# Performance work log

Hardware: AMD Instinct MI355X
Metric: run time of the kernel (lower is better)

Reference implementation:

```python
import jax, jax.numpy as jnp
import numpy as np

N_E, FEAT, REST = 2048, 512, 8
HEAD, LENGTH = 8, 64


def setup_inputs() -> dict:
    key = jax.random.key(0)
    kx, kq, kk, kd = jax.random.split(key, 4)
    x = jax.random.normal(kx, (N_E, FEAT, REST), dtype=jnp.float32)
    Q = jax.random.normal(kq, (HEAD, LENGTH, FEAT), dtype=jnp.float32)
    K = jax.random.normal(kk, (HEAD, LENGTH, FEAT), dtype=jnp.float32)
    D = jax.random.normal(kd, (HEAD, LENGTH, FEAT), dtype=jnp.float32)
    return {"x": x, "Q": Q, "K": K, "D": D}


def _linear(a, W):
    # a: (n, f, *rest), W: (h, q, f) -> y: (n, h, q, *rest)
    y = jnp.einsum('nf...,hqf->nhq...', a, W)
    # L2-normalize over the last 3 axes (here: h? no -- axes (q, rest...) per the
    # original code: sum over (-1,-2,-3) of (n,h,q,rest) = (h,q,rest) per n)
    norm = jnp.sqrt((y * y).sum((-1, -2, -3), keepdims=True))
    return y / norm


def reference(x, Q, K, D):
    n_e = x.shape[0]
    rest = x.shape[2:]
    head, length = Q.shape[0], Q.shape[1]
    q = _linear(x, Q)  # (n, h, l, rest)
    k = _linear(x, K)
    d = _linear(x, D)
    # scores over electrons: contract (l, rest) -> (h, n, n)
    w = jax.nn.softmax(jnp.einsum('nh...,mh...->hnm', q, k), axis=-1)
    # weighted combine: (h,n,m) x (m,h,l,rest) -> (n,h,l,rest)
    v = jnp.einsum('hnm,mhl...->nhl...', w, d)
    return v.reshape((n_e, head * length) + rest)
```

## Files before the change

kernel.cpp:

```cpp
#include <hip/hip_runtime.h>
#include <math.h>

#define NE   2048
#define FEAT 512

typedef short short8 __attribute__((ext_vector_type(8)));
typedef float f32x4  __attribute__((ext_vector_type(4)));

__device__ __forceinline__ unsigned short f2bf(float f) {
    union { float f; unsigned u; } v; v.f = f;
    unsigned r = v.u + 0x7fffu + ((v.u >> 16) & 1u);
    return (unsigned short)(r >> 16);
}
__device__ __forceinline__ float bf2f(unsigned b) {
    union { unsigned u; float f; } v; v.u = b << 16;
    return v.f;
}
__device__ __forceinline__ unsigned pack2(float a, float b) {
    return (unsigned)f2bf(a) | ((unsigned)f2bf(b) << 16);
}

__device__ __forceinline__ void gld16(unsigned short* lds, const unsigned short* g) {
    __builtin_amdgcn_global_load_lds(
        (const __attribute__((address_space(1))) unsigned int*)g,
        (__attribute__((address_space(3))) unsigned int*)lds,
        16, 0, 0);
}

__device__ __forceinline__ void bar() {
    asm volatile("" ::: "memory");
    __builtin_amdgcn_s_barrier();
    asm volatile("" ::: "memory");
}
#define VMW(n) asm volatile("s_waitcnt vmcnt(" #n ")" ::: "memory")


__global__ __launch_bounds__(256) void wconv_kernel(
    const float* __restrict__ Wq, const float* __restrict__ Wk, const float* __restrict__ Wd,
    unsigned short* __restrict__ wbf)
{
    const int t = threadIdx.x;
    const float* W = (blockIdx.y == 0) ? Wq : (blockIdx.y == 1) ? Wk : Wd;
    unsigned short* o = wbf + (size_t)blockIdx.y * 262144;
    const int idx = blockIdx.x * 2048 + t * 8;
    const float4* p = (const float4*)(W + idx);
    float4 v0 = p[0], v1 = p[1];
    *(uint4*)(o + idx) = make_uint4(pack2(v0.x, v0.y), pack2(v0.z, v0.w),
                                    pack2(v1.x, v1.y), pack2(v1.z, v1.w));
}

__global__ __launch_bounds__(256) void xpose_kernel(const float* __restrict__ x,
                                                    unsigned short* __restrict__ xt)
{
    __shared__ float xs[8 * 516];
    const int t = threadIdx.x;
    const int n = blockIdx.x;
    const float4* xp = (const float4*)(x + (size_t)n * 4096);
    #pragma unroll
    for (int i = 0; i < 4; ++i) {
        int idx = t + 256 * i;
        float4 v = xp[idx];
        int f = idx >> 1, rh = (idx & 1) * 4;
        xs[(rh + 0) * 516 + f] = v.x;
        xs[(rh + 1) * 516 + f] = v.y;
        xs[(rh + 2) * 516 + f] = v.z;
        xs[(rh + 3) * 516 + f] = v.w;
    }
    __syncthreads();
    const int r = t >> 5, f0 = (t & 31) * 16;
    const float* src = &xs[r * 516 + f0];
    unsigned o[8];
    #pragma unroll
    for (int j = 0; j < 8; ++j) o[j] = pack2(src[2 * j], src[2 * j + 1]);
    unsigned short* dst = xt + (size_t)n * 4096 + r * 512 + f0;
    *(uint4*)dst       = make_uint4(o[0], o[1], o[2], o[3]);
    *(uint4*)(dst + 8) = make_uint4(o[4], o[5], o[6], o[7]);
}

__global__ __launch_bounds__(512, 1) void proj_gemm(
    const unsigned short* __restrict__ wbf, const unsigned short* __restrict__ xt,
    unsigned short* __restrict__ qb, unsigned short* __restrict__ kb, unsigned short* __restrict__ db,
    float* __restrict__ s2)
{
    __shared__ unsigned short SM[49152];
    const int t = threadIdx.x;
    int bid = blockIdx.x + 128 * (blockIdx.y + 2 * blockIdx.z);
    int swz = (bid & 7) * 96 + (bid >> 3);
    const int bx = swz & 127, rest = swz >> 7;
    const int my = rest & 1, w = rest >> 1;
    const unsigned short* W = wbf + (size_t)w * 262144;
    unsigned short* out = (w == 0) ? qb : (w == 1) ? kb : db;
    const int M0 = my * 256;
    const int N0 = bx * 128;
    const int wave = t >> 6, lane = t & 63, quad = lane >> 4, l16 = lane & 15;
    const int wr = wave >> 1, wc = wave & 1;
    const int lrow = lane >> 3;
    const int scol = ((lane & 7) ^ lrow) * 8;

    f32x4 acc[4][4];
    #pragma unroll
    for (int m = 0; m < 4; ++m)
        #pragma unroll
        for (int n = 0; n < 4; ++n) acc[m][n] = {0.f, 0.f, 0.f, 0.f};

    auto STAGE = [&](int kc, int buf) {
        unsigned short* A = SM + buf * 16384;
        unsigned short* B = SM + 32768 + buf * 8192;
        #pragma unroll
        for (int p = 0; p < 4; ++p) {
            int c = p * 8 + wave;
            gld16(A + c * 512, W + (size_t)(M0 + c * 8 + lrow) * 512 + kc * 64 + scol);
        }
        #pragma unroll
        for (int p = 0; p < 2; ++p) {
            int c = p * 8 + wave;
            gld16(B + c * 512, xt + (size_t)(N0 + c * 8 + lrow) * 512 + kc * 64 + scol);
        }
    };
    auto COMPUTE = [&](int buf) {
        const unsigned short* A = SM + buf * 16384;
        const unsigned short* B = SM + 32768 + buf * 8192;
        #pragma unroll
        for (int kk = 0; kk < 2; ++kk) {
            int so = ((kk * 4 + quad) ^ (l16 & 7)) * 8;
            short8 a[4], b[4];
            #pragma unroll
            for (int m = 0; m < 4; ++m)
                a[m] = *(const short8*)&A[(wr * 64 + m * 16 + l16) * 64 + so];
            #pragma unroll
            for (int n = 0; n < 4; ++n)
                b[n] = *(const short8*)&B[(wc * 64 + n * 16 + l16) * 64 + so];
            #pragma unroll
            for (int m = 0; m < 4; ++m)
                #pragma unroll
                for (int n = 0; n < 4; ++n)
                    acc[m][n] = __builtin_amdgcn_mfma_f32_16x16x32_bf16(a[m], b[n], acc[m][n], 0, 0, 0);
        }
    };

    STAGE(0, 0);
    STAGE(1, 1);
    for (int kc = 0; kc < 8; ++kc) {
        if (kc < 7) { VMW(6); } else { VMW(0); }
        bar();
        COMPUTE(kc & 1);
        bar();
        if (kc + 2 < 8) STAGE(kc + 2, kc & 1);
    }

    float cs[4];
    #pragma unroll
    for (int n = 0; n < 4; ++n) {
        float s = 0.f;
        #pragma unroll
        for (int m = 0; m < 4; ++m)
            #pragma unroll
            for (int reg = 0; reg < 4; ++reg)
                s += acc[m][n][reg] * acc[m][n][reg];
        cs[n] = s;
    }
    #pragma unroll
    for (int n = 0; n < 4; ++n) {
        float s = cs[n];
        s += __shfl_xor(s, 16);
        s += __shfl_xor(s, 32);
        s += __shfl_xor(s, 1);
        s += __shfl_xor(s, 2);
        s += __shfl_xor(s, 4);
        if ((lane & 7) == 0 && lane < 16) {
            int n_elec = (N0 >> 3) + wc * 8 + n * 2 + (lane >> 3);
            atomicAdd(&s2[w * NE + n_elec], s);
        }
    }

    unsigned short* T = SM;
    #pragma unroll
    for (int m = 0; m < 4; ++m)
        #pragma unroll
        for (int reg = 0; reg < 4; ++reg) {
            int row = wr * 64 + m * 16 + quad * 4 + reg;
            #pragma unroll
            for (int n = 0; n < 4; ++n)
                T[row * 136 + wc * 64 + n * 16 + l16] = f2bf(acc[m][n][reg]);
        }
    __syncthreads();
    #pragma unroll
    for (int i = 0; i < 8; ++i) {
        int c = t + 512 * i;
        int row = c & 255, cb = c >> 8;
        uint4 v = *(const uint4*)(T + row * 136 + cb * 8);
        int hl = M0 + row;
        unsigned short* dst = out + (size_t)(hl >> 6) * 1048576 + (size_t)(hl & 63) * 8
                                  + (size_t)((N0 >> 3) + cb) * 512;
        *(uint4*)dst = v;
    }
}

__global__ __launch_bounds__(256) void sfinal_kernel(const float* __restrict__ s2,
                                                     float* __restrict__ scales)
{
    int i = blockIdx.x * 256 + threadIdx.x;
    scales[i] = rsqrtf(s2[i]);
}

__global__ __launch_bounds__(256) void dtrans_kernel(
    const unsigned short* __restrict__ db, const float* __restrict__ invd,
    unsigned short* __restrict__ dT)
{
    __shared__ float Ts[64 * 68];
    const int t = threadIdx.x;
    const int h = blockIdx.z, n0 = blockIdx.y * 64, f0 = blockIdx.x * 64;
    const int rr = t >> 3, cs = (t & 7) * 8;
    #pragma unroll
    for (int p = 0; p < 2; ++p) {
        int row = rr + p * 32;
        float sc = invd[n0 + row];
        uint4 v = *(const uint4*)(db + ((size_t)h * NE + n0 + row) * 512 + f0 + cs);
        unsigned a[4] = {v.x, v.y, v.z, v.w};
        float* d = &Ts[row * 68 + cs];
        #pragma unroll
        for (int j = 0; j < 4; ++j) {
            d[2 * j]     = bf2f(a[j] & 0xffffu) * sc;
            d[2 * j + 1] = bf2f(a[j] >> 16) * sc;
        }
    }
    __syncthreads();
    const int f = t >> 2, ns = (t & 3) * 16;
    unsigned o[8];
    #pragma unroll
    for (int j = 0; j < 8; ++j)
        o[j] = pack2(Ts[(ns + 2 * j) * 68 + f], Ts[(ns + 2 * j + 1) * 68 + f]);
    unsigned short* dst = dT + ((size_t)h * 512 + f0 + f) * NE + n0 + ns;
    *(uint4*)dst       = make_uint4(o[0], o[1], o[2], o[3]);
    *(uint4*)(dst + 8) = make_uint4(o[4], o[5], o[6], o[7]);
}

__global__ __launch_bounds__(512, 2) void score_kernel(
    const unsigned short* __restrict__ qb, const unsigned short* __restrict__ kb,
    const float* __restrict__ scales, unsigned short* __restrict__ P,
    float* __restrict__ sums, int g)
{
    __shared__ unsigned short SM[65536];
    const int t = threadIdx.x;
    int bid = blockIdx.x + 8 * (blockIdx.y + 8 * blockIdx.z);
    int swz = (bid & 7) * 32 + (bid >> 3);
    const int bx = swz & 7, by = (swz >> 3) & 7, bz = swz >> 6;
    const int hg = bz, h = g * 4 + hg;
    const int n0 = by * 256, m0 = bx * 256;
    const int wave = t >> 6, lane = t & 63, quad = lane >> 4, l16 = lane & 15;
    const int wr = wave >> 2, wc = wave & 3;
    const int lrow = lane >> 3;
    const int scol = ((lane & 7) ^ lrow) * 8;
    const unsigned short* qh = qb + (size_t)h * NE * 512;
    const unsigned short* kh = kb + (size_t)h * NE * 512;

    f32x4 acc[8][4];
    #pragma unroll
    for (int m = 0; m < 8; ++m)
        #pragma unroll
        for (int n = 0; n < 4; ++n) acc[m][n] = {0.f, 0.f, 0.f, 0.f};

    auto STAGE = [&](int kc, int buf) {
        unsigned short* A = SM + buf * 16384;
        unsigned short* B = SM + 32768 + buf * 16384;
        #pragma unroll
        for (int p = 0; p < 4; ++p) {
            int c = p * 8 + wave;
            gld16(A + c * 512, qh + (size_t)(n0 + c * 8 + lrow) * 512 + kc * 64 + scol);
        }
        #pragma unroll
        for (int p = 0; p < 4; ++p) {
            int c = p * 8 + wave;
            gld16(B + c * 512, kh + (size_t)(m0 + c * 8 + lrow) * 512 + kc * 64 + scol);
        }
    };
    auto COMPUTE = [&](int buf) {
        const unsigned short* A = SM + buf * 16384;
        const unsigned short* B = SM + 32768 + buf * 16384;
        #pragma unroll
        for (int kk = 0; kk < 2; ++kk) {
            int so = ((kk * 4 + quad) ^ (l16 & 7)) * 8;
            short8 a[8], b[4];
            #pragma unroll
            for (int m = 0; m < 8; ++m)
                a[m] = *(const short8*)&A[(wr * 128 + m * 16 + l16) * 64 + so];
            #pragma unroll
            for (int n = 0; n < 4; ++n)
                b[n] = *(const short8*)&B[(wc * 64 + n * 16 + l16) * 64 + so];
            #pragma unroll
            for (int m = 0; m < 8; ++m)
                #pragma unroll
                for (int n = 0; n < 4; ++n)
                    acc[m][n] = __builtin_amdgcn_mfma_f32_16x16x32_bf16(a[m], b[n], acc[m][n], 0, 0, 0);
        }
    };

    STAGE(0, 0);
    STAGE(1, 1);
    for (int kc = 0; kc < 8; ++kc) {
        if (kc < 7) { VMW(8); } else { VMW(0); }
        bar();
        COMPUTE(kc & 1);
        bar();
        if (kc + 2 < 8) STAGE(kc + 2, kc & 1);
    }

    float ik[4];
    #pragma unroll
    for (int n = 0; n < 4; ++n) ik[n] = scales[NE + m0 + wc * 64 + n * 16 + l16];

    unsigned short* Ph = P + (size_t)hg * NE * NE;
    #pragma unroll
    for (int m = 0; m < 8; ++m)
        #pragma unroll
        for (int reg = 0; reg < 4; ++reg) {
            int row = n0 + wr * 128 + m * 16 + quad * 4 + reg;
            float qs = scales[row];
            unsigned short* prow = Ph + (size_t)row * NE + m0 + wc * 64;
            float rs = 0.f;
            #pragma unroll
            for (int n = 0; n < 4; ++n) {
                float e = __expf(acc[m][n][reg] * qs * ik[n]);
                unsigned short bx16 = f2bf(e);
                prow[n * 16 + l16] = bx16;
                rs += bf2f(bx16);
            }
            rs += __shfl_xor(rs, 1);
            rs += __shfl_xor(rs, 2);
            rs += __shfl_xor(rs, 4);
            rs += __shfl_xor(rs, 8);
            if (l16 == 0) atomicAdd(&sums[hg * NE + row], rs);
        }
}

__global__ __launch_bounds__(512) void combine_kernel(
    const unsigned short* __restrict__ P, const unsigned short* __restrict__ dT,
    const float* __restrict__ sums, float* __restrict__ out, int g)
{
    __shared__ unsigned short Ps[8192];
    __shared__ unsigned short Ds[8192];
    const int t = threadIdx.x;
    int bid = blockIdx.x + 4 * (blockIdx.y + 16 * blockIdx.z);
    int swz = (bid & 7) * 32 + (bid >> 3);
    const int bx = swz & 3, by = (swz >> 2) & 15, bz = swz >> 6;
    const int hg = bz, h = g * 4 + hg;
    const int n0 = by * 128, f0 = bx * 128;
    const int wave = t >> 6, lane = t & 63, quad = lane >> 4, l16 = lane & 15;
    const int wn = wave >> 1, wf = wave & 1;
    const int lrow = lane >> 3;
    const int scol = ((lane & 7) ^ lrow) * 8;
    const unsigned short* Ph = P + (size_t)hg * NE * NE;
    const unsigned short* dh = dT + (size_t)h * 512 * NE;

    f32x4 acc[2][4];
    #pragma unroll
    for (int i = 0; i < 2; ++i)
        #pragma unroll
        for (int j = 0; j < 4; ++j) acc[i][j] = {0.f, 0.f, 0.f, 0.f};

    for (int mc = 0; mc < 32; ++mc) {
        #pragma unroll
        for (int p = 0; p < 2; ++p) {
            int c = p * 8 + wave;
            gld16(Ps + c * 512, Ph + (size_t)(n0 + c * 8 + lrow) * NE + mc * 64 + scol);
            gld16(Ds + c * 512, dh + (size_t)(f0 + c * 8 + lrow) * NE + mc * 64 + scol);
        }
        __syncthreads();
        #pragma unroll
        for (int kk = 0; kk < 2; ++kk) {
            int so = ((kk * 4 + quad) ^ (l16 & 7)) * 8;
            short8 a0 = *(const short8*)&Ps[(wn * 32 + l16) * 64 + so];
            short8 a1 = *(const short8*)&Ps[(wn * 32 + 16 + l16) * 64 + so];
            #pragma unroll
            for (int ct = 0; ct < 4; ++ct) {
                short8 bb = *(const short8*)&Ds[(wf * 64 + ct * 16 + l16) * 64 + so];
                acc[0][ct] = __builtin_amdgcn_mfma_f32_16x16x32_bf16(a0, bb, acc[0][ct], 0, 0, 0);
                acc[1][ct] = __builtin_amdgcn_mfma_f32_16x16x32_bf16(a1, bb, acc[1][ct], 0, 0, 0);
            }
        }
        __syncthreads();
    }

    #pragma unroll
    for (int rt = 0; rt < 2; ++rt)
        #pragma unroll
        for (int reg = 0; reg < 4; ++reg) {
            int nl = wn * 32 + rt * 16 + quad * 4 + reg;
            float li = 1.0f / sums[hg * NE + n0 + nl];
            float* orow = out + (size_t)(n0 + nl) * 4096 + h * 512 + f0 + wf * 64;
            #pragma unroll
            for (int ct = 0; ct < 4; ++ct)
                orow[ct * 16 + l16] = acc[rt][ct][reg] * li;
        }
}

extern "C" void kernel_launch(void* const* d_in, const int* in_sizes, int n_in,
                              void* d_out, int out_size, void* d_ws, size_t ws_size,
                              hipStream_t stream)
{
    const float* x  = (const float*)d_in[0];
    const float* Qw = (const float*)d_in[1];
    const float* Kw = (const float*)d_in[2];
    const float* Dw = (const float*)d_in[3];
    float* out = (float*)d_out;

    char* ws = (char*)d_ws;
    unsigned short* xt = (unsigned short*)ws;
    unsigned short* db = (unsigned short*)(ws + 16777216);
    unsigned short* P  = (unsigned short*)ws;
    unsigned short* qb = (unsigned short*)(ws + 33554432);
    unsigned short* kb = (unsigned short*)(ws + 33554432 + 16777216);
    unsigned short* dT = (unsigned short*)(ws + 33554432 + 2 * 16777216);
    unsigned short* wbf = dT;
    float* scales = (float*)(ws + 83886080);
    float* sums   = (float*)(ws + 83886080 + 24576);
    float* s2     = (float*)(ws + 83886080 + 24576 + 32768);

    wconv_kernel<<<dim3(128, 3), 256, 0, stream>>>(Qw, Kw, Dw, wbf);
    xpose_kernel<<<2048, 256, 0, stream>>>(x, xt);
    hipMemsetAsync(s2, 0, 3 * NE * sizeof(float), stream);
    proj_gemm<<<dim3(128, 2, 3), 512, 0, stream>>>(wbf, xt, qb, kb, db, s2);
    sfinal_kernel<<<24, 256, 0, stream>>>(s2, scales);
    dtrans_kernel<<<dim3(8, 32, 8), 256, 0, stream>>>(db, scales + 2 * NE, dT);
    for (int g = 0; g < 2; ++g) {
        hipMemsetAsync(sums, 0, 4 * NE * sizeof(float), stream);
        score_kernel<<<dim3(8, 8, 4), 512, 0, stream>>>(qb, kb, scales, P, sums, g);
        combine_kernel<<<dim3(4, 16, 4), 512, 0, stream>>>(P, dT, sums, out, g);
    }
}
```

Before: 281.7 us.

## Shrink score tiles, stage P through LDS, double-buffer combine loads

```diff
diff --git a/kernel.cpp b/kernel.cpp
--- a/kernel.cpp
+++ b/kernel.cpp
@@ -235,110 +235,102 @@
     *(uint4*)(dst + 8) = make_uint4(o[4], o[5], o[6], o[7]);
 }
 
-__global__ __launch_bounds__(512, 2) void score_kernel(
+__global__ __launch_bounds__(256) void score_kernel(
     const unsigned short* __restrict__ qb, const unsigned short* __restrict__ kb,
     const float* __restrict__ scales, unsigned short* __restrict__ P,
     float* __restrict__ sums, int g)
 {
-    __shared__ unsigned short SM[65536];
-    const int t = threadIdx.x;
-    int bid = blockIdx.x + 8 * (blockIdx.y + 8 * blockIdx.z);
-    int swz = (bid & 7) * 32 + (bid >> 3);
-    const int bx = swz & 7, by = (swz >> 3) & 7, bz = swz >> 6;
+    __shared__ unsigned short SM[17408];
+    const int t = threadIdx.x;
+    int bid = blockIdx.x + 16 * (blockIdx.y + 16 * blockIdx.z);
+    int swz = (bid & 7) * 128 + (bid >> 3);
+    const int bx = swz & 15, by = (swz >> 4) & 15, bz = swz >> 8;
     const int hg = bz, h = g * 4 + hg;
-    const int n0 = by * 256, m0 = bx * 256;
+    const int n0 = by * 128, m0 = bx * 128;
     const int wave = t >> 6, lane = t & 63, quad = lane >> 4, l16 = lane & 15;
-    const int wr = wave >> 2, wc = wave & 3;
     const int lrow = lane >> 3;
     const int scol = ((lane & 7) ^ lrow) * 8;
     const unsigned short* qh = qb + (size_t)h * NE * 512;
     const unsigned short* kh = kb + (size_t)h * NE * 512;
-
-    f32x4 acc[8][4];
-    #pragma unroll
-    for (int m = 0; m < 8; ++m)
-        #pragma unroll
-        for (int n = 0; n < 4; ++n) acc[m][n] = {0.f, 0.f, 0.f, 0.f};
-
-    auto STAGE = [&](int kc, int buf) {
-        unsigned short* A = SM + buf * 16384;
-        unsigned short* B = SM + 32768 + buf * 16384;
+    unsigned short* As = SM;
+    unsigned short* Bs = SM + 8192;
+
+    f32x4 acc[2][8];
+    #pragma unroll
+    for (int i = 0; i < 2; ++i)
+        #pragma unroll
+        for (int j = 0; j < 8; ++j) acc[i][j] = {0.f, 0.f, 0.f, 0.f};
+
+    for (int kc = 0; kc < 8; ++kc) {
         #pragma unroll
         for (int p = 0; p < 4; ++p) {
-            int c = p * 8 + wave;
-            gld16(A + c * 512, qh + (size_t)(n0 + c * 8 + lrow) * 512 + kc * 64 + scol);
-        }
-        #pragma unroll
-        for (int p = 0; p < 4; ++p) {
-            int c = p * 8 + wave;
-            gld16(B + c * 512, kh + (size_t)(m0 + c * 8 + lrow) * 512 + kc * 64 + scol);
-        }
-    };
-    auto COMPUTE = [&](int buf) {
-        const unsigned short* A = SM + buf * 16384;
-        const unsigned short* B = SM + 32768 + buf * 16384;
+            int c = p * 4 + wave;
+            gld16(As + c * 512, qh + (size_t)(n0 + c * 8 + lrow) * 512 + kc * 64 + scol);
+            gld16(Bs + c * 512, kh + (size_t)(m0 + c * 8 + lrow) * 512 + kc * 64 + scol);
+        }
+        __syncthreads();
         #pragma unroll
         for (int kk = 0; kk < 2; ++kk) {
             int so = ((kk * 4 + quad) ^ (l16 & 7)) * 8;
-            short8 a[8], b[4];
-            #pragma unroll
-            for (int m = 0; m < 8; ++m)
-                a[m] = *(const short8*)&A[(wr * 128 + m * 16 + l16) * 64 + so];
-            #pragma unroll
-            for (int n = 0; n < 4; ++n)
-                b[n] = *(const short8*)&B[(wc * 64 + n * 16 + l16) * 64 + so];
-            #pragma unroll
-            for (int m = 0; m < 8; ++m)
-                #pragma unroll
-                for (int n = 0; n < 4; ++n)
-                    acc[m][n] = __builtin_amdgcn_mfma_f32_16x16x32_bf16(a[m], b[n], acc[m][n], 0, 0, 0);
-        }
-    };
-
-    STAGE(0, 0);
-    STAGE(1, 1);
-    for (int kc = 0; kc < 8; ++kc) {
-        if (kc < 7) { VMW(8); } else { VMW(0); }
-        bar();
-        COMPUTE(kc & 1);
-        bar();
-        if (kc + 2 < 8) STAGE(kc + 2, kc & 1);
-    }
-
-    float ik[4];
-    #pragma unroll
-    for (int n = 0; n < 4; ++n) ik[n] = scales[NE + m0 + wc * 64 + n * 16 + l16];
-
-    unsigned short* Ph = P + (size_t)hg * NE * NE;
-    #pragma unroll
-    for (int m = 0; m < 8; ++m)
+            short8 a0 = *(const short8*)&As[(wave * 32 + l16) * 64 + so];
+            short8 a1 = *(const short8*)&As[(wave * 32 + 16 + l16) * 64 + so];
+            #pragma unroll
+            for (int ct = 0; ct < 8; ++ct) {
+                short8 bb = *(const short8*)&Bs[(ct * 16 + l16) * 64 + so];
+                acc[0][ct] = __builtin_amdgcn_mfma_f32_16x16x32_bf16(a0, bb, acc[0][ct], 0, 0, 0);
+                acc[1][ct] = __builtin_amdgcn_mfma_f32_16x16x32_bf16(a1, bb, acc[1][ct], 0, 0, 0);
+            }
+        }
+        __syncthreads();
+    }
+
+    float iq[2][4], ik[8];
+    #pragma unroll
+    for (int rt = 0; rt < 2; ++rt)
+        #pragma unroll
+        for (int reg = 0; reg < 4; ++reg)
+            iq[rt][reg] = scales[n0 + wave * 32 + rt * 16 + quad * 4 + reg];
+    #pragma unroll
+    for (int ct = 0; ct < 8; ++ct) ik[ct] = scales[NE + m0 + ct * 16 + l16];
+
+    unsigned short* T = SM;
+    #pragma unroll
+    for (int rt = 0; rt < 2; ++rt)
         #pragma unroll
         for (int reg = 0; reg < 4; ++reg) {
-            int row = n0 + wr * 128 + m * 16 + quad * 4 + reg;
-            float qs = scales[row];
-            unsigned short* prow = Ph + (size_t)row * NE + m0 + wc * 64;
+            int nl = wave * 32 + rt * 16 + quad * 4 + reg;
+            float qs = iq[rt][reg];
             float rs = 0.f;
             #pragma unroll
-            for (int n = 0; n < 4; ++n) {
-                float e = __expf(acc[m][n][reg] * qs * ik[n]);
+            for (int ct = 0; ct < 8; ++ct) {
+                float e = __expf(acc[rt][ct][reg] * qs * ik[ct]);
                 unsigned short bx16 = f2bf(e);
-                prow[n * 16 + l16] = bx16;
+                T[nl * 136 + ct * 16 + l16] = bx16;
                 rs += bf2f(bx16);
             }
             rs += __shfl_xor(rs, 1);
             rs += __shfl_xor(rs, 2);
             rs += __shfl_xor(rs, 4);
             rs += __shfl_xor(rs, 8);
-            if (l16 == 0) atomicAdd(&sums[hg * NE + row], rs);
-        }
+            if (l16 == 0) atomicAdd(&sums[hg * NE + n0 + nl], rs);
+        }
+    __syncthreads();
+    unsigned short* Ph = P + (size_t)hg * NE * NE;
+    #pragma unroll
+    for (int i = 0; i < 8; ++i) {
+        int c = t + 256 * i;
+        int row = c >> 4, cb = c & 15;
+        uint4 v = *(const uint4*)(T + row * 136 + cb * 8);
+        *(uint4*)(Ph + (size_t)(n0 + row) * NE + m0 + cb * 8) = v;
+    }
 }
 
 __global__ __launch_bounds__(512) void combine_kernel(
     const unsigned short* __restrict__ P, const unsigned short* __restrict__ dT,
     const float* __restrict__ sums, float* __restrict__ out, int g)
 {
-    __shared__ unsigned short Ps[8192];
-    __shared__ unsigned short Ds[8192];
+    __shared__ unsigned short Ps[2][8192];
+    __shared__ unsigned short Ds[2][8192];
     const int t = threadIdx.x;
     int bid = blockIdx.x + 4 * (blockIdx.y + 16 * blockIdx.z);
     int swz = (bid & 7) * 32 + (bid >> 3);
@@ -358,27 +350,37 @@
         #pragma unroll
         for (int j = 0; j < 4; ++j) acc[i][j] = {0.f, 0.f, 0.f, 0.f};
 
-    for (int mc = 0; mc < 32; ++mc) {
+    auto STAGE = [&](int mc, int buf) {
         #pragma unroll
         for (int p = 0; p < 2; ++p) {
             int c = p * 8 + wave;
-            gld16(Ps + c * 512, Ph + (size_t)(n0 + c * 8 + lrow) * NE + mc * 64 + scol);
-            gld16(Ds + c * 512, dh + (size_t)(f0 + c * 8 + lrow) * NE + mc * 64 + scol);
-        }
-        __syncthreads();
+            gld16(&Ps[buf][c * 512], Ph + (size_t)(n0 + c * 8 + lrow) * NE + mc * 64 + scol);
+            gld16(&Ds[buf][c * 512], dh + (size_t)(f0 + c * 8 + lrow) * NE + mc * 64 + scol);
+        }
+    };
+    auto COMPUTE = [&](int buf) {
         #pragma unroll
         for (int kk = 0; kk < 2; ++kk) {
             int so = ((kk * 4 + quad) ^ (l16 & 7)) * 8;
-            short8 a0 = *(const short8*)&Ps[(wn * 32 + l16) * 64 + so];
-            short8 a1 = *(const short8*)&Ps[(wn * 32 + 16 + l16) * 64 + so];
+            short8 a0 = *(const short8*)&Ps[buf][(wn * 32 + l16) * 64 + so];
+            short8 a1 = *(const short8*)&Ps[buf][(wn * 32 + 16 + l16) * 64 + so];
             #pragma unroll
             for (int ct = 0; ct < 4; ++ct) {
-                short8 bb = *(const short8*)&Ds[(wf * 64 + ct * 16 + l16) * 64 + so];
+                short8 bb = *(const short8*)&Ds[buf][(wf * 64 + ct * 16 + l16) * 64 + so];
                 acc[0][ct] = __builtin_amdgcn_mfma_f32_16x16x32_bf16(a0, bb, acc[0][ct], 0, 0, 0);
                 acc[1][ct] = __builtin_amdgcn_mfma_f32_16x16x32_bf16(a1, bb, acc[1][ct], 0, 0, 0);
             }
         }
-        __syncthreads();
+    };
+
+    STAGE(0, 0);
+    STAGE(1, 1);
+    for (int mc = 0; mc < 32; ++mc) {
+        if (mc < 31) { VMW(4); } else { VMW(0); }
+        bar();
+        COMPUTE(mc & 1);
+        bar();
+        if (mc + 2 < 32) STAGE(mc + 2, mc & 1);
     }
 
     #pragma unroll
@@ -424,7 +426,7 @@
     dtrans_kernel<<<dim3(8, 32, 8), 256, 0, stream>>>(db, scales + 2 * NE, dT);
     for (int g = 0; g < 2; ++g) {
         hipMemsetAsync(sums, 0, 4 * NE * sizeof(float), stream);
-        score_kernel<<<dim3(8, 8, 4), 512, 0, stream>>>(qb, kb, scales, P, sums, g);
+        score_kernel<<<dim3(16, 16, 4), 256, 0, stream>>>(qb, kb, scales, P, sums, g);
         combine_kernel<<<dim3(4, 16, 4), 512, 0, stream>>>(P, dT, sums, out, g);
     }
 }
```

New measurement: 266.1 us. 1.06x faster.

## Shrink score tiles, stage P through LDS, double-buffer combine loads

Applied to the files above, without the earlier changes.

```diff
diff --git a/kernel.cpp b/kernel.cpp
--- a/kernel.cpp
+++ b/kernel.cpp
@@ -235,60 +235,60 @@
     *(uint4*)(dst + 8) = make_uint4(o[4], o[5], o[6], o[7]);
 }
 
-__global__ __launch_bounds__(512, 2) void score_kernel(
+__global__ __launch_bounds__(512, 1) void score_kernel(
     const unsigned short* __restrict__ qb, const unsigned short* __restrict__ kb,
     const float* __restrict__ scales, unsigned short* __restrict__ P,
     float* __restrict__ sums, int g)
 {
-    __shared__ unsigned short SM[65536];
-    const int t = threadIdx.x;
-    int bid = blockIdx.x + 8 * (blockIdx.y + 8 * blockIdx.z);
-    int swz = (bid & 7) * 32 + (bid >> 3);
-    const int bx = swz & 7, by = (swz >> 3) & 7, bz = swz >> 6;
+    __shared__ unsigned short SM[49152];
+    const int t = threadIdx.x;
+    int bid = blockIdx.x + 16 * (blockIdx.y + 8 * blockIdx.z);
+    int swz = (bid & 7) * 64 + (bid >> 3);
+    const int bx = swz & 15, by = (swz >> 4) & 7, bz = swz >> 7;
     const int hg = bz, h = g * 4 + hg;
-    const int n0 = by * 256, m0 = bx * 256;
+    const int n0 = by * 256, m0 = bx * 128;
     const int wave = t >> 6, lane = t & 63, quad = lane >> 4, l16 = lane & 15;
-    const int wr = wave >> 2, wc = wave & 3;
+    const int wr = wave >> 1, wc = wave & 1;
     const int lrow = lane >> 3;
     const int scol = ((lane & 7) ^ lrow) * 8;
     const unsigned short* qh = qb + (size_t)h * NE * 512;
     const unsigned short* kh = kb + (size_t)h * NE * 512;
 
-    f32x4 acc[8][4];
-    #pragma unroll
-    for (int m = 0; m < 8; ++m)
+    f32x4 acc[4][4];
+    #pragma unroll
+    for (int m = 0; m < 4; ++m)
         #pragma unroll
         for (int n = 0; n < 4; ++n) acc[m][n] = {0.f, 0.f, 0.f, 0.f};
 
     auto STAGE = [&](int kc, int buf) {
         unsigned short* A = SM + buf * 16384;
-        unsigned short* B = SM + 32768 + buf * 16384;
+        unsigned short* B = SM + 32768 + buf * 8192;
         #pragma unroll
         for (int p = 0; p < 4; ++p) {
             int c = p * 8 + wave;
             gld16(A + c * 512, qh + (size_t)(n0 + c * 8 + lrow) * 512 + kc * 64 + scol);
         }
         #pragma unroll
-        for (int p = 0; p < 4; ++p) {
+        for (int p = 0; p < 2; ++p) {
             int c = p * 8 + wave;
             gld16(B + c * 512, kh + (size_t)(m0 + c * 8 + lrow) * 512 + kc * 64 + scol);
         }
     };
     auto COMPUTE = [&](int buf) {
         const unsigned short* A = SM + buf * 16384;
-        const unsigned short* B = SM + 32768 + buf * 16384;
+        const unsigned short* B = SM + 32768 + buf * 8192;
         #pragma unroll
         for (int kk = 0; kk < 2; ++kk) {
             int so = ((kk * 4 + quad) ^ (l16 & 7)) * 8;
-            short8 a[8], b[4];
-            #pragma unroll
-            for (int m = 0; m < 8; ++m)
-                a[m] = *(const short8*)&A[(wr * 128 + m * 16 + l16) * 64 + so];
+            short8 a[4], b[4];
+            #pragma unroll
+            for (int m = 0; m < 4; ++m)
+                a[m] = *(const short8*)&A[(wr * 64 + m * 16 + l16) * 64 + so];
             #pragma unroll
             for (int n = 0; n < 4; ++n)
                 b[n] = *(const short8*)&B[(wc * 64 + n * 16 + l16) * 64 + so];
             #pragma unroll
-            for (int m = 0; m < 8; ++m)
+            for (int m = 0; m < 4; ++m)
                 #pragma unroll
                 for (int n = 0; n < 4; ++n)
                     acc[m][n] = __builtin_amdgcn_mfma_f32_16x16x32_bf16(a[m], b[n], acc[m][n], 0, 0, 0);
@@ -298,7 +298,7 @@
     STAGE(0, 0);
     STAGE(1, 1);
     for (int kc = 0; kc < 8; ++kc) {
-        if (kc < 7) { VMW(8); } else { VMW(0); }
+        if (kc < 7) { VMW(6); } else { VMW(0); }
         bar();
         COMPUTE(kc & 1);
         bar();
@@ -309,36 +309,44 @@
     #pragma unroll
     for (int n = 0; n < 4; ++n) ik[n] = scales[NE + m0 + wc * 64 + n * 16 + l16];
 
-    unsigned short* Ph = P + (size_t)hg * NE * NE;
-    #pragma unroll
-    for (int m = 0; m < 8; ++m)
+    unsigned short* T = SM;
+    #pragma unroll
+    for (int m = 0; m < 4; ++m)
         #pragma unroll
         for (int reg = 0; reg < 4; ++reg) {
-            int row = n0 + wr * 128 + m * 16 + quad * 4 + reg;
-            float qs = scales[row];
-            unsigned short* prow = Ph + (size_t)row * NE + m0 + wc * 64;
+            int row = wr * 64 + m * 16 + quad * 4 + reg;
+            float qs = scales[n0 + row];
             float rs = 0.f;
             #pragma unroll
             for (int n = 0; n < 4; ++n) {
                 float e = __expf(acc[m][n][reg] * qs * ik[n]);
                 unsigned short bx16 = f2bf(e);
-                prow[n * 16 + l16] = bx16;
+                T[row * 136 + wc * 64 + n * 16 + l16] = bx16;
                 rs += bf2f(bx16);
             }
             rs += __shfl_xor(rs, 1);
             rs += __shfl_xor(rs, 2);
             rs += __shfl_xor(rs, 4);
             rs += __shfl_xor(rs, 8);
-            if (l16 == 0) atomicAdd(&sums[hg * NE + row], rs);
-        }
+            if (l16 == 0) atomicAdd(&sums[hg * NE + n0 + row], rs);
+        }
+    __syncthreads();
+    unsigned short* Ph = P + (size_t)hg * NE * NE;
+    #pragma unroll
+    for (int i = 0; i < 8; ++i) {
+        int c = t + 512 * i;
+        int row = c >> 4, cb = c & 15;
+        uint4 v = *(const uint4*)(T + row * 136 + cb * 8);
+        *(uint4*)(Ph + (size_t)(n0 + row) * NE + m0 + cb * 8) = v;
+    }
 }
 
 __global__ __launch_bounds__(512) void combine_kernel(
     const unsigned short* __restrict__ P, const unsigned short* __restrict__ dT,
     const float* __restrict__ sums, float* __restrict__ out, int g)
 {
-    __shared__ unsigned short Ps[8192];
-    __shared__ unsigned short Ds[8192];
+    __shared__ unsigned short Ps[2][8192];
+    __shared__ unsigned short Ds[2][8192];
     const int t = threadIdx.x;
     int bid = blockIdx.x + 4 * (blockIdx.y + 16 * blockIdx.z);
     int swz = (bid & 7) * 32 + (bid >> 3);
@@ -358,27 +366,37 @@
         #pragma unroll
         for (int j = 0; j < 4; ++j) acc[i][j] = {0.f, 0.f, 0.f, 0.f};
 
-    for (int mc = 0; mc < 32; ++mc) {
+    auto STAGE = [&](int mc, int buf) {
         #pragma unroll
         for (int p = 0; p < 2; ++p) {
             int c = p * 8 + wave;
-            gld16(Ps + c * 512, Ph + (size_t)(n0 + c * 8 + lrow) * NE + mc * 64 + scol);
-            gld16(Ds + c * 512, dh + (size_t)(f0 + c * 8 + lrow) * NE + mc * 64 + scol);
-        }
-        __syncthreads();
+            gld16(&Ps[buf][c * 512], Ph + (size_t)(n0 + c * 8 + lrow) * NE + mc * 64 + scol);
+            gld16(&Ds[buf][c * 512], dh + (size_t)(f0 + c * 8 + lrow) * NE + mc * 64 + scol);
+        }
+    };
+    auto COMPUTE = [&](int buf) {
         #pragma unroll
         for (int kk = 0; kk < 2; ++kk) {
             int so = ((kk * 4 + quad) ^ (l16 & 7)) * 8;
-            short8 a0 = *(const short8*)&Ps[(wn * 32 + l16) * 64 + so];
-            short8 a1 = *(const short8*)&Ps[(wn * 32 + 16 + l16) * 64 + so];
+            short8 a0 = *(const short8*)&Ps[buf][(wn * 32 + l16) * 64 + so];
+            short8 a1 = *(const short8*)&Ps[buf][(wn * 32 + 16 + l16) * 64 + so];
             #pragma unroll
             for (int ct = 0; ct < 4; ++ct) {
-                short8 bb = *(const short8*)&Ds[(wf * 64 + ct * 16 + l16) * 64 + so];
+                short8 bb = *(const short8*)&Ds[buf][(wf * 64 + ct * 16 + l16) * 64 + so];
                 acc[0][ct] = __builtin_amdgcn_mfma_f32_16x16x32_bf16(a0, bb, acc[0][ct], 0, 0, 0);
                 acc[1][ct] = __builtin_amdgcn_mfma_f32_16x16x32_bf16(a1, bb, acc[1][ct], 0, 0, 0);
             }
         }
-        __syncthreads();
+    };
+
+    STAGE(0, 0);
+    STAGE(1, 1);
+    for (int mc = 0; mc < 32; ++mc) {
+        if (mc < 31) { VMW(4); } else { VMW(0); }
+        bar();
+        COMPUTE(mc & 1);
+        bar();
+        if (mc + 2 < 32) STAGE(mc + 2, mc & 1);
     }
 
     #pragma unroll
@@ -424,7 +442,7 @@
     dtrans_kernel<<<dim3(8, 32, 8), 256, 0, stream>>>(db, scales + 2 * NE, dT);
     for (int g = 0; g < 2; ++g) {
         hipMemsetAsync(sums, 0, 4 * NE * sizeof(float), stream);
-        score_kernel<<<dim3(8, 8, 4), 512, 0, stream>>>(qb, kb, scales, P, sums, g);
+        score_kernel<<<dim3(16, 8, 4), 512, 0, stream>>>(qb, kb, scales, P, sums, g);
         combine_kernel<<<dim3(4, 16, 4), 512, 0, stream>>>(P, dT, sums, out, g);
     }
 }
```

Result: faster. 271.7 us (-3.5%).
